# Performance work log

Hardware: AMD Instinct MI355X
Metric: run time of the kernel (lower is better)

The kernel has to match this reference:

```python
import jax, jax.numpy as jnp
import numpy as np

NQ = 10          # num_qubits
NL = 4           # num_layers (StronglyEntanglingLayers)
DIM = 2 ** NQ    # state-vector dimension = input_linear out features
B = 4096
SEQ = 512
PRED = 96

# ---- static basis-state bookkeeping (wire 0 = most significant bit, as in PennyLane) ----

def _cnot_perm(control, target):
    s = np.arange(DIM)
    bit = (s >> (NQ - 1 - control)) & 1
    return s ^ (bit << (NQ - 1 - target))

def _layer_perms():
    # StronglyEntanglingLayers default ranges: r_l = (l % (n_wires - 1)) + 1,
    # then CNOT(i, (i+r) % n) for i = 0..n-1, applied sequentially.
    perms = []
    for l in range(NL):
        r = (l % (NQ - 1)) + 1
        comp = np.arange(DIM)
        for c in range(NQ):
            g = _cnot_perm(c, (c + r) % NQ)
            comp = comp[g]          # compose: state_new[t] = state_old[comp[t]]
        perms.append(jnp.asarray(comp))
    return perms

PERMS = _layer_perms()

_bits = (np.arange(DIM)[:, None] >> (NQ - 1 - np.arange(NQ))[None, :]) & 1
SIGNS = jnp.asarray(1.0 - 2.0 * _bits, dtype=np.float32)   # [DIM, NQ] PauliZ eigenvalues


def _rot_gates(w):
    # PennyLane Rot(phi, theta, omega) = RZ(omega) @ RY(theta) @ RZ(phi); w: [L, n, 3]
    phi, theta, omega = w[..., 0], w[..., 1], w[..., 2]
    c = jnp.cos(theta / 2)
    s = jnp.sin(theta / 2)
    ep = jnp.exp(0.5j * (phi + omega))   # e^{+i(phi+omega)/2}
    em = jnp.exp(0.5j * (phi - omega))   # e^{+i(phi-omega)/2}
    m00 = jnp.conj(ep) * c
    m01 = -em * s
    m10 = jnp.conj(em) * s
    m11 = ep * c
    return jnp.stack([jnp.stack([m00, m01], -1),
                      jnp.stack([m10, m11], -1)], -2)       # [L, n, 2, 2] complex64


def _apply_1q(psi, U, wire):
    # psi: [B, DIM] complex; apply 2x2 U on `wire`
    b = psi.shape[0]
    left = 2 ** wire
    right = 2 ** (NQ - 1 - wire)
    psi = psi.reshape(b, left, 2, right)
    psi = jnp.einsum('ba,kpaq->kpbq', U, psi)
    return psi.reshape(b, DIM)


def _circuit(psi, q_weights):
    mats = _rot_gates(q_weights)
    for l in range(NL):
        for w in range(NQ):
            psi = _apply_1q(psi, mats[l, w], w)
        psi = psi[:, PERMS[l]]          # composed CNOT ring of this layer
    return psi


def reference(x, W_in, b_in, q_weights, W_out, b_out):
    h = x @ W_in.T + b_in + 1e-6                          # input_linear, then +1e-6
    norm = jnp.linalg.norm(h, axis=-1, keepdims=True)
    psi = (h / norm).astype(jnp.complex64)                # AmplitudeEmbedding(normalize=True)
    psi = _circuit(psi, q_weights)                        # StronglyEntanglingLayers
    probs = psi.real ** 2 + psi.imag ** 2
    expvals = probs @ SIGNS                               # [B, NQ] PauliZ expvals
    return expvals @ W_out.T + b_out                      # output_linear


def setup_inputs() -> dict:
    key = jax.random.key(0)
    ks = jax.random.split(key, 6)
    x = jax.random.normal(ks[0], (B, SEQ), dtype=jnp.float32)
    W_in = jax.random.normal(ks[1], (DIM, SEQ), dtype=jnp.float32) / np.sqrt(SEQ)
    b_in = jax.random.normal(ks[2], (DIM,), dtype=jnp.float32) * 0.01
    q_weights = jax.random.uniform(ks[3], (NL, NQ, 3), dtype=jnp.float32,
                                   minval=0.0, maxval=2.0 * np.pi)
    W_out = jax.random.normal(ks[4], (PRED, NQ), dtype=jnp.float32) / np.sqrt(NQ)
    b_out = jax.random.normal(ks[5], (PRED,), dtype=jnp.float32) * 0.01
    return {"x": x, "W_in": W_in, "b_in": b_in, "q_weights": q_weights,
            "W_out": W_out, "b_out": b_out}
```

## Files before the change

### kernel.cpp

```cpp
#include <hip/hip_runtime.h>
#include <math.h>

#define DIM 1024
#define NQ 10
#define NL 4
#define SEQ 512
#define NROWS 4096
#define PRED 96

typedef unsigned short ushort_t;
typedef unsigned int uint_t;
using short8  = __attribute__((ext_vector_type(8))) short;
using float4v = __attribute__((ext_vector_type(4))) float;

__device__ inline uint_t f2bf1(float f) {
    uint_t u = __float_as_uint(f);
    return (u + 0x7fffu + ((u >> 16) & 1u)) >> 16;
}
__device__ inline float bf2f(uint_t s) { return __uint_as_float(s << 16); }

__global__ __launch_bounds__(512)
void circuit_cols_kernel(const float* __restrict__ Wi, const float* __restrict__ b_in,
                         const float* __restrict__ qw,
                         ushort_t* __restrict__ Crt_r, ushort_t* __restrict__ Crt_i,
                         float* __restrict__ dr, float* __restrict__ di)
{
    __shared__ float2 psi[DIM];
    __shared__ float gm[NL * NQ][8];

    const int tid = threadIdx.x;
    const int j = blockIdx.x;

    if (tid < NL * NQ) {
        float phi = qw[tid * 3 + 0], theta = qw[tid * 3 + 1], omega = qw[tid * 3 + 2];
        float ch = cosf(theta * 0.5f), sh = sinf(theta * 0.5f);
        float a = 0.5f * (phi + omega), b = 0.5f * (phi - omega);
        float ca = cosf(a), sa = sinf(a);
        float cb = cosf(b), sb = sinf(b);
        gm[tid][0] =  ch * ca;  gm[tid][1] = -ch * sa;
        gm[tid][2] = -sh * cb;  gm[tid][3] = -sh * sb;
        gm[tid][4] =  sh * cb;  gm[tid][5] = -sh * sb;
        gm[tid][6] =  ch * ca;  gm[tid][7] =  ch * sa;
    }

    float v0, v1;
    if (j < SEQ) {
        v0 = Wi[(size_t)(2 * tid) * SEQ + j];
        v1 = Wi[(size_t)(2 * tid + 1) * SEQ + j];
    } else {
        v0 = b_in[2 * tid] + 1e-6f;
        v1 = b_in[2 * tid + 1] + 1e-6f;
    }
    psi[2 * tid]     = make_float2(v0, 0.f);
    psi[2 * tid + 1] = make_float2(v1, 0.f);
    __syncthreads();

    for (int l = 0; l < NL; ++l) {
#pragma unroll
        for (int w = 0; w < NQ; ++w) {
            const float* m = gm[l * NQ + w];
            float m00r = m[0], m00i = m[1], m01r = m[2], m01i = m[3];
            float m10r = m[4], m10i = m[5], m11r = m[6], m11i = m[7];
            int mask = 1 << (9 - w);
            int lo = tid & (mask - 1);
            int s0 = ((tid ^ lo) << 1) | lo;
            int s1 = s0 | mask;
            float2 a0 = psi[s0], a1 = psi[s1];
            float2 n0, n1;
            n0.x = m00r * a0.x - m00i * a0.y + m01r * a1.x - m01i * a1.y;
            n0.y = m00r * a0.y + m00i * a0.x + m01r * a1.y + m01i * a1.x;
            n1.x = m10r * a0.x - m10i * a0.y + m11r * a1.x - m11i * a1.y;
            n1.y = m10r * a0.y + m10i * a0.x + m11r * a1.y + m11i * a1.x;
            psi[s0] = n0; psi[s1] = n1;
            __syncthreads();
        }
        int r = l % (NQ - 1) + 1;
        int p0 = tid, p1 = tid + 512;
#pragma unroll
        for (int c = 9; c >= 0; --c) {
            int t = (c + r) % NQ;
            p0 ^= ((p0 >> (9 - c)) & 1) << (9 - t);
            p1 ^= ((p1 >> (9 - c)) & 1) << (9 - t);
        }
        float2 t0 = psi[p0], t1 = psi[p1];
        __syncthreads();
        psi[tid] = t0; psi[tid + 512] = t1;
        __syncthreads();
    }

    float2 o0 = psi[tid], o1 = psi[tid + 512];
    if (j < SEQ) {
        Crt_r[(size_t)tid * SEQ + j]         = (ushort_t)f2bf1(o0.x);
        Crt_i[(size_t)tid * SEQ + j]         = (ushort_t)f2bf1(o0.y);
        Crt_r[(size_t)(tid + 512) * SEQ + j] = (ushort_t)f2bf1(o1.x);
        Crt_i[(size_t)(tid + 512) * SEQ + j] = (ushort_t)f2bf1(o1.y);
    } else {
        dr[tid] = o0.x;        di[tid] = o0.y;
        dr[tid + 512] = o1.x;  di[tid + 512] = o1.y;
    }
}

#define GBM 128
#define GBNC 64
#define GBK 32
#define LDA 40
#define LDP 65

__global__ __launch_bounds__(256)
void gemm_fused_kernel(const float* __restrict__ x,
                       const ushort_t* __restrict__ Crt_r, const ushort_t* __restrict__ Crt_i,
                       const float* __restrict__ dr, const float* __restrict__ di,
                       float* __restrict__ part)
{
    __shared__ __align__(16) char lds[GBM * LDP * 4];
    ushort_t* Ash = (ushort_t*)lds;
    ushort_t* Asl = Ash + GBM * LDA;
    ushort_t* Bsr = Asl + GBM * LDA;
    ushort_t* Bsi = Bsr + GBNC * LDA;
    float*    Ps  = (float*)lds;
    __shared__ float drs[GBNC], dis[GBNC];

    const int tid = threadIdx.x;
    const int bm = blockIdx.x, bn = blockIdx.y;
    const int lane = tid & 63, wv = tid >> 6;
    const int n0 = bn * GBNC;

    if (tid < GBNC) { drs[tid] = dr[n0 + tid]; dis[tid] = di[n0 + tid]; }

    float4v accr[2][4], acci[2][4];
#pragma unroll
    for (int a = 0; a < 2; ++a)
#pragma unroll
        for (int b = 0; b < 4; ++b) { accr[a][b] = (float4v)0.f; acci[a][b] = (float4v)0.f; }

    const int sr = tid >> 1, ko = (tid & 1) * 16;
    const float* xa = x + (size_t)(bm * GBM + sr) * SEQ + ko;
    const int bsel = tid >> 7;
    const int nr = (tid & 127) >> 1;
    const int bko = (tid & 1) * 16;
    const ushort_t* bsrc = (bsel ? Crt_i : Crt_r) + (size_t)(n0 + nr) * SEQ + bko;
    ushort_t* bdst = (bsel ? Bsi : Bsr) + nr * LDA + bko;

    const int fm = lane & 15, kq = (lane >> 4) * 8;
    const int wrow = wv * 32;

    for (int k0 = 0; k0 < SEQ; k0 += GBK) {
        float fv[16];
        *(float4*)&fv[0]  = *(const float4*)(xa + k0);
        *(float4*)&fv[4]  = *(const float4*)(xa + k0 + 4);
        *(float4*)&fv[8]  = *(const float4*)(xa + k0 + 8);
        *(float4*)&fv[12] = *(const float4*)(xa + k0 + 12);
        uint_t ph[8], pl[8];
#pragma unroll
        for (int i = 0; i < 8; ++i) {
            uint_t h0 = f2bf1(fv[2 * i]), h1 = f2bf1(fv[2 * i + 1]);
            float l0 = fv[2 * i] - bf2f(h0), l1 = fv[2 * i + 1] - bf2f(h1);
            ph[i] = h0 | (h1 << 16);
            pl[i] = f2bf1(l0) | (f2bf1(l1) << 16);
        }
        *(uint4*)(Ash + sr * LDA + ko)     = make_uint4(ph[0], ph[1], ph[2], ph[3]);
        *(uint4*)(Ash + sr * LDA + ko + 8) = make_uint4(ph[4], ph[5], ph[6], ph[7]);
        *(uint4*)(Asl + sr * LDA + ko)     = make_uint4(pl[0], pl[1], pl[2], pl[3]);
        *(uint4*)(Asl + sr * LDA + ko + 8) = make_uint4(pl[4], pl[5], pl[6], pl[7]);
        uint4 b0 = *(const uint4*)(bsrc + k0);
        uint4 b1 = *(const uint4*)(bsrc + k0 + 8);
        *(uint4*)bdst       = b0;
        *(uint4*)(bdst + 8) = b1;
        __syncthreads();

        short8 ah0 = *(short8*)(Ash + (wrow + fm) * LDA + kq);
        short8 ah1 = *(short8*)(Ash + (wrow + 16 + fm) * LDA + kq);
        short8 al0 = *(short8*)(Asl + (wrow + fm) * LDA + kq);
        short8 al1 = *(short8*)(Asl + (wrow + 16 + fm) * LDA + kq);
#pragma unroll
        for (int nt = 0; nt < 4; ++nt) {
            short8 br = *(short8*)(Bsr + (nt * 16 + fm) * LDA + kq);
            short8 bi = *(short8*)(Bsi + (nt * 16 + fm) * LDA + kq);
            accr[0][nt] = __builtin_amdgcn_mfma_f32_16x16x32_bf16(ah0, br, accr[0][nt], 0, 0, 0);
            accr[1][nt] = __builtin_amdgcn_mfma_f32_16x16x32_bf16(ah1, br, accr[1][nt], 0, 0, 0);
            acci[0][nt] = __builtin_amdgcn_mfma_f32_16x16x32_bf16(ah0, bi, acci[0][nt], 0, 0, 0);
            acci[1][nt] = __builtin_amdgcn_mfma_f32_16x16x32_bf16(ah1, bi, acci[1][nt], 0, 0, 0);
            accr[0][nt] = __builtin_amdgcn_mfma_f32_16x16x32_bf16(al0, br, accr[0][nt], 0, 0, 0);
            accr[1][nt] = __builtin_amdgcn_mfma_f32_16x16x32_bf16(al1, br, accr[1][nt], 0, 0, 0);
            acci[0][nt] = __builtin_amdgcn_mfma_f32_16x16x32_bf16(al0, bi, acci[0][nt], 0, 0, 0);
            acci[1][nt] = __builtin_amdgcn_mfma_f32_16x16x32_bf16(al1, bi, acci[1][nt], 0, 0, 0);
        }
        __syncthreads();
    }

    const int rq = (lane >> 4) * 4;
#pragma unroll
    for (int mt = 0; mt < 2; ++mt)
#pragma unroll
        for (int nt = 0; nt < 4; ++nt) {
            float drv = drs[nt * 16 + fm], div = dis[nt * 16 + fm];
#pragma unroll
            for (int reg = 0; reg < 4; ++reg) {
                int lrow = wrow + mt * 16 + rq + reg;
                float zr = accr[mt][nt][reg] + drv;
                float zi = acci[mt][nt][reg] + div;
                Ps[lrow * LDP + nt * 16 + fm] = zr * zr + zi * zi;
            }
        }
    __syncthreads();

    {
        const int row = tid >> 1, hh = tid & 1;
        const float* pr = Ps + row * LDP + hh * 32;
        float nrm = 0.f, e0 = 0.f, e1 = 0.f, e2 = 0.f, e3 = 0.f, e4 = 0.f, e5 = 0.f;
#pragma unroll
        for (int i = 0; i < 32; ++i) {
            float p = pr[i];
            int c = hh * 32 + i;
            nrm += p;
            e0 += ((c >> 5) & 1) ? -p : p;
            e1 += ((c >> 4) & 1) ? -p : p;
            e2 += ((c >> 3) & 1) ? -p : p;
            e3 += ((c >> 2) & 1) ? -p : p;
            e4 += ((c >> 1) & 1) ? -p : p;
            e5 += (c & 1) ? -p : p;
        }
        size_t base = ((size_t)(bn * 2 + hh) * NROWS + bm * GBM + row) * 8;
        part[base + 0] = nrm;
        part[base + 1] = e0; part[base + 2] = e1; part[base + 3] = e2;
        part[base + 4] = e3; part[base + 5] = e4; part[base + 6] = e5;
    }
}

__global__ __launch_bounds__(128)
void finalize_kernel(const float* __restrict__ part, const float* __restrict__ W_out,
                     const float* __restrict__ b_out, float* __restrict__ out)
{
    __shared__ float sred[32][8];
    __shared__ float evf[12];
    const int row = blockIdx.x, tid = threadIdx.x;

    if (tid < 32) {
        const float* p = part + ((size_t)tid * NROWS + row) * 8;
        *(float4*)&sred[tid][0] = *(const float4*)p;
        *(float4*)&sred[tid][4] = *(const float4*)(p + 4);
    }
    __syncthreads();
    if (tid == 0) {
        float nrm = 0.f, ev[10];
#pragma unroll
        for (int k = 0; k < 10; ++k) ev[k] = 0.f;
        for (int pb = 0; pb < 32; ++pb) {
            int bnn = pb >> 1;
            float n0 = sred[pb][0];
            nrm += n0;
            ev[0] += ((bnn >> 3) & 1) ? -n0 : n0;
            ev[1] += ((bnn >> 2) & 1) ? -n0 : n0;
            ev[2] += ((bnn >> 1) & 1) ? -n0 : n0;
            ev[3] += (bnn & 1) ? -n0 : n0;
#pragma unroll
            for (int k = 4; k < 10; ++k) ev[k] += sred[pb][k - 3];
        }
        float inv = 1.0f / nrm;
#pragma unroll
        for (int k = 0; k < 10; ++k) evf[k] = ev[k] * inv;
    }
    __syncthreads();
    if (tid < PRED) {
        float o = b_out[tid];
#pragma unroll
        for (int k = 0; k < NQ; ++k) o = fmaf(W_out[tid * NQ + k], evf[k], o);
        out[(size_t)row * PRED + tid] = o;
    }
}

extern "C" void kernel_launch(void* const* d_in, const int* in_sizes, int n_in,
                              void* d_out, int out_size, void* d_ws, size_t ws_size,
                              hipStream_t stream) {
    const float* x     = (const float*)d_in[0];
    const float* W_in  = (const float*)d_in[1];
    const float* b_in  = (const float*)d_in[2];
    const float* qw    = (const float*)d_in[3];
    const float* W_out = (const float*)d_in[4];
    const float* b_out = (const float*)d_in[5];
    float* out = (float*)d_out;

    char* w = (char*)d_ws;
    ushort_t* Crt_r = (ushort_t*)w;
    ushort_t* Crt_i = (ushort_t*)(w + (1u << 20));
    float* dr = (float*)(w + 2 * (1u << 20));
    float* di = dr + DIM;
    float* part = (float*)(w + 3 * (1u << 20));

    circuit_cols_kernel<<<SEQ + 1, 512, 0, stream>>>(W_in, b_in, qw, Crt_r, Crt_i, dr, di);
    dim3 g2(NROWS / GBM, DIM / GBNC);
    gemm_fused_kernel<<<g2, 256, 0, stream>>>(x, Crt_r, Crt_i, dr, di, part);
    finalize_kernel<<<NROWS, 128, 0, stream>>>(part, W_out, b_out, out);
}
```

Measured before the change: 122.0 us.

## Switch input GEMM from split-bf16 to single fp16 MFMA and shuffle-reduce finalize

Replaces the two-term bf16 hi/lo split of x (which doubled the MFMA count and A-tile LDS traffic) with a single fp16 conversion and fp16 MFMAs, and stores the circuit columns as fp16. This halves the tensor-core work and removes the residual computation, at the cost of reduced precision (fp16 range and mantissa) on x and the circuit matrix. The partial-sum layout is also transposed so each output row's partials are contiguous. The finalize kernel now reduces them with wave shuffles instead of a single-thread serial loop.

```diff
diff --git a/kernel.cpp b/kernel.cpp
--- a/kernel.cpp
+++ b/kernel.cpp
@@ -10,14 +10,14 @@
 
 typedef unsigned short ushort_t;
 typedef unsigned int uint_t;
-using short8  = __attribute__((ext_vector_type(8))) short;
+using half8   = __attribute__((ext_vector_type(8))) _Float16;
 using float4v = __attribute__((ext_vector_type(4))) float;
 
-__device__ inline uint_t f2bf1(float f) {
-    uint_t u = __float_as_uint(f);
-    return (u + 0x7fffu + ((u >> 16) & 1u)) >> 16;
-}
-__device__ inline float bf2f(uint_t s) { return __uint_as_float(s << 16); }
+__device__ inline ushort_t f2h(float f) { _Float16 h = (_Float16)f; return *(ushort_t*)&h; }
+__device__ inline uint_t pkh(float a, float b) {
+    _Float16 ha = (_Float16)a, hb = (_Float16)b;
+    return (uint_t)(*(ushort_t*)&ha) | ((uint_t)(*(ushort_t*)&hb) << 16);
+}
 
 __global__ __launch_bounds__(512)
 void circuit_cols_kernel(const float* __restrict__ Wi, const float* __restrict__ b_in,
@@ -90,10 +90,10 @@
 
     float2 o0 = psi[tid], o1 = psi[tid + 512];
     if (j < SEQ) {
-        Crt_r[(size_t)tid * SEQ + j]         = (ushort_t)f2bf1(o0.x);
-        Crt_i[(size_t)tid * SEQ + j]         = (ushort_t)f2bf1(o0.y);
-        Crt_r[(size_t)(tid + 512) * SEQ + j] = (ushort_t)f2bf1(o1.x);
-        Crt_i[(size_t)(tid + 512) * SEQ + j] = (ushort_t)f2bf1(o1.y);
+        Crt_r[(size_t)tid * SEQ + j]         = f2h(o0.x);
+        Crt_i[(size_t)tid * SEQ + j]         = f2h(o0.y);
+        Crt_r[(size_t)(tid + 512) * SEQ + j] = f2h(o1.x);
+        Crt_i[(size_t)(tid + 512) * SEQ + j] = f2h(o1.y);
     } else {
         dr[tid] = o0.x;        di[tid] = o0.y;
         dr[tid + 512] = o1.x;  di[tid + 512] = o1.y;
@@ -114,8 +114,7 @@
 {
     __shared__ __align__(16) char lds[GBM * LDP * 4];
     ushort_t* Ash = (ushort_t*)lds;
-    ushort_t* Asl = Ash + GBM * LDA;
-    ushort_t* Bsr = Asl + GBM * LDA;
+    ushort_t* Bsr = Ash + GBM * LDA;
     ushort_t* Bsi = Bsr + GBNC * LDA;
     float*    Ps  = (float*)lds;
     __shared__ float drs[GBNC], dis[GBNC];
@@ -150,40 +149,27 @@
         *(float4*)&fv[4]  = *(const float4*)(xa + k0 + 4);
         *(float4*)&fv[8]  = *(const float4*)(xa + k0 + 8);
         *(float4*)&fv[12] = *(const float4*)(xa + k0 + 12);
-        uint_t ph[8], pl[8];
-#pragma unroll
-        for (int i = 0; i < 8; ++i) {
-            uint_t h0 = f2bf1(fv[2 * i]), h1 = f2bf1(fv[2 * i + 1]);
-            float l0 = fv[2 * i] - bf2f(h0), l1 = fv[2 * i + 1] - bf2f(h1);
-            ph[i] = h0 | (h1 << 16);
-            pl[i] = f2bf1(l0) | (f2bf1(l1) << 16);
-        }
-        *(uint4*)(Ash + sr * LDA + ko)     = make_uint4(ph[0], ph[1], ph[2], ph[3]);
-        *(uint4*)(Ash + sr * LDA + ko + 8) = make_uint4(ph[4], ph[5], ph[6], ph[7]);
-        *(uint4*)(Asl + sr * LDA + ko)     = make_uint4(pl[0], pl[1], pl[2], pl[3]);
-        *(uint4*)(Asl + sr * LDA + ko + 8) = make_uint4(pl[4], pl[5], pl[6], pl[7]);
+        uint_t pk[8];
+#pragma unroll
+        for (int i = 0; i < 8; ++i) pk[i] = pkh(fv[2 * i], fv[2 * i + 1]);
+        *(uint4*)(Ash + sr * LDA + ko)     = make_uint4(pk[0], pk[1], pk[2], pk[3]);
+        *(uint4*)(Ash + sr * LDA + ko + 8) = make_uint4(pk[4], pk[5], pk[6], pk[7]);
         uint4 b0 = *(const uint4*)(bsrc + k0);
         uint4 b1 = *(const uint4*)(bsrc + k0 + 8);
         *(uint4*)bdst       = b0;
         *(uint4*)(bdst + 8) = b1;
         __syncthreads();
 
-        short8 ah0 = *(short8*)(Ash + (wrow + fm) * LDA + kq);
-        short8 ah1 = *(short8*)(Ash + (wrow + 16 + fm) * LDA + kq);
-        short8 al0 = *(short8*)(Asl + (wrow + fm) * LDA + kq);
-        short8 al1 = *(short8*)(Asl + (wrow + 16 + fm) * LDA + kq);
+        half8 ah0 = *(half8*)(Ash + (wrow + fm) * LDA + kq);
+        half8 ah1 = *(half8*)(Ash + (wrow + 16 + fm) * LDA + kq);
 #pragma unroll
         for (int nt = 0; nt < 4; ++nt) {
-            short8 br = *(short8*)(Bsr + (nt * 16 + fm) * LDA + kq);
-            short8 bi = *(short8*)(Bsi + (nt * 16 + fm) * LDA + kq);
-            accr[0][nt] = __builtin_amdgcn_mfma_f32_16x16x32_bf16(ah0, br, accr[0][nt], 0, 0, 0);
-            accr[1][nt] = __builtin_amdgcn_mfma_f32_16x16x32_bf16(ah1, br, accr[1][nt], 0, 0, 0);
-            acci[0][nt] = __builtin_amdgcn_mfma_f32_16x16x32_bf16(ah0, bi, acci[0][nt], 0, 0, 0);
-            acci[1][nt] = __builtin_amdgcn_mfma_f32_16x16x32_bf16(ah1, bi, acci[1][nt], 0, 0, 0);
-            accr[0][nt] = __builtin_amdgcn_mfma_f32_16x16x32_bf16(al0, br, accr[0][nt], 0, 0, 0);
-            accr[1][nt] = __builtin_amdgcn_mfma_f32_16x16x32_bf16(al1, br, accr[1][nt], 0, 0, 0);
-            acci[0][nt] = __builtin_amdgcn_mfma_f32_16x16x32_bf16(al0, bi, acci[0][nt], 0, 0, 0);
-            acci[1][nt] = __builtin_amdgcn_mfma_f32_16x16x32_bf16(al1, bi, acci[1][nt], 0, 0, 0);
+            half8 br = *(half8*)(Bsr + (nt * 16 + fm) * LDA + kq);
+            half8 bi = *(half8*)(Bsi + (nt * 16 + fm) * LDA + kq);
+            accr[0][nt] = __builtin_amdgcn_mfma_f32_16x16x32_f16(ah0, br, accr[0][nt], 0, 0, 0);
+            accr[1][nt] = __builtin_amdgcn_mfma_f32_16x16x32_f16(ah1, br, accr[1][nt], 0, 0, 0);
+            acci[0][nt] = __builtin_amdgcn_mfma_f32_16x16x32_f16(ah0, bi, acci[0][nt], 0, 0, 0);
+            acci[1][nt] = __builtin_amdgcn_mfma_f32_16x16x32_f16(ah1, bi, acci[1][nt], 0, 0, 0);
         }
         __syncthreads();
     }
@@ -220,7 +206,7 @@
             e4 += ((c >> 1) & 1) ? -p : p;
             e5 += (c & 1) ? -p : p;
         }
-        size_t base = ((size_t)(bn * 2 + hh) * NROWS + bm * GBM + row) * 8;
+        size_t base = ((size_t)(bm * GBM + row) * 32 + (bn * 2 + hh)) * 8;
         part[base + 0] = nrm;
         part[base + 1] = e0; part[base + 2] = e1; part[base + 3] = e2;
         part[base + 4] = e3; part[base + 5] = e4; part[base + 6] = e5;
@@ -231,34 +217,37 @@
 void finalize_kernel(const float* __restrict__ part, const float* __restrict__ W_out,
                      const float* __restrict__ b_out, float* __restrict__ out)
 {
-    __shared__ float sred[32][8];
-    __shared__ float evf[12];
+    __shared__ float evf[16];
     const int row = blockIdx.x, tid = threadIdx.x;
 
-    if (tid < 32) {
-        const float* p = part + ((size_t)tid * NROWS + row) * 8;
-        *(float4*)&sred[tid][0] = *(const float4*)p;
-        *(float4*)&sred[tid][4] = *(const float4*)(p + 4);
-    }
-    __syncthreads();
-    if (tid == 0) {
-        float nrm = 0.f, ev[10];
-#pragma unroll
-        for (int k = 0; k < 10; ++k) ev[k] = 0.f;
-        for (int pb = 0; pb < 32; ++pb) {
-            int bnn = pb >> 1;
-            float n0 = sred[pb][0];
-            nrm += n0;
-            ev[0] += ((bnn >> 3) & 1) ? -n0 : n0;
-            ev[1] += ((bnn >> 2) & 1) ? -n0 : n0;
-            ev[2] += ((bnn >> 1) & 1) ? -n0 : n0;
-            ev[3] += (bnn & 1) ? -n0 : n0;
-#pragma unroll
-            for (int k = 4; k < 10; ++k) ev[k] += sred[pb][k - 3];
-        }
-        float inv = 1.0f / nrm;
-#pragma unroll
-        for (int k = 0; k < 10; ++k) evf[k] = ev[k] * inv;
+    if (tid < 64) {
+        float v[11];
+        if (tid < 32) {
+            const float* p = part + ((size_t)row * 32 + tid) * 8;
+            float4 a = *(const float4*)p;
+            float4 b = *(const float4*)(p + 4);
+            float nrm = a.x;
+            int bnn = tid >> 1;
+            v[0] = nrm;
+            v[1] = (bnn & 8) ? -nrm : nrm;
+            v[2] = (bnn & 4) ? -nrm : nrm;
+            v[3] = (bnn & 2) ? -nrm : nrm;
+            v[4] = (bnn & 1) ? -nrm : nrm;
+            v[5] = a.y; v[6] = a.z; v[7] = a.w;
+            v[8] = b.x; v[9] = b.y; v[10] = b.z;
+        } else {
+#pragma unroll
+            for (int k = 0; k < 11; ++k) v[k] = 0.f;
+        }
+#pragma unroll
+        for (int m = 16; m; m >>= 1)
+#pragma unroll
+            for (int k = 0; k < 11; ++k) v[k] += __shfl_xor(v[k], m, 64);
+        if (tid == 0) {
+            float inv = 1.0f / v[0];
+#pragma unroll
+            for (int k = 0; k < 10; ++k) evf[k] = v[k + 1] * inv;
+        }
     }
     __syncthreads();
     if (tid < PRED) {
```

Result: faster. 114.7 us (-6.0%).
